# Kernel tuning notes

Hardware: AMD Instinct MI355X
Metric: run time of the kernel (lower is better)

Reference implementation:

```python
import jax, jax.numpy as jnp
import numpy as np

B, N, N_HEAD, HDIM = 16, 512, 8, 64


def setup_inputs() -> dict:
    key = jax.random.key(0)
    kq, kk, kv, kg = jax.random.split(key, 4)
    q = jax.random.normal(kq, (B, N, N_HEAD, HDIM), dtype=jnp.float32)
    k = jax.random.normal(kk, (B, N, N_HEAD, HDIM), dtype=jnp.float32)
    v = jax.random.normal(kv, (B, N, N_HEAD, HDIM), dtype=jnp.float32)
    geo_f = jax.random.normal(kg, (B, N, N), dtype=jnp.float32)
    return {"q": q, "k": k, "v": v, "geo_f": geo_f}


def reference(q, k, v, geo_f):
    # q,k,v: [B,N,H,D]; geo_f: [B,N,N]
    D = q.shape[-1]
    scale = D ** (-0.5)  # total_weight = qk_weight / scale  (i.e. * sqrt(D))
    # pairwise_distance = negative squared Euclidean distance between per-head
    # query/key vectors: -||q_i - k_j||^2 = 2 q.k - ||q||^2 - ||k||^2
    qk = jnp.einsum('bnhd,bmhd->bhnm', q, k)            # [B,H,N,N]
    q2 = jnp.sum(q * q, axis=-1).transpose(0, 2, 1)     # [B,H,N]
    k2 = jnp.sum(k * k, axis=-1).transpose(0, 2, 1)     # [B,H,N]
    dist = 2.0 * qk - q2[..., :, None] - k2[..., None, :]
    total = (dist + geo_f[:, None, :, :]) / scale       # geo bias broadcast over heads
    # global max subtraction in the source is a no-op under softmax; softmax is stable anyway
    w = jax.nn.softmax(total, axis=-1)                  # [B,H,N,N]
    # weighted sum over keys m (dropout p=0.0 -> identity)
    out = jnp.einsum('bmhd,bhnm->bnhd', v, w)           # [B,N,H,D]
    return out
```

## Files before the change

kernel.cpp:

```cpp
#include <hip/hip_runtime.h>
#include <hip/hip_bf16.h>

#define BB 16
#define NN 512
#define NH 8
#define DD 64
#define CK 64
#define NCH 8
#define TL 4
#define MWAVES 8
#define MQBLK 128
#define QBLK 64
#define WAVES 4
#define KBLK 128
#define NCHUNK 4
#define NT 32
#define TPC 8

typedef __attribute__((ext_vector_type(8))) short bf16x8;
typedef __attribute__((ext_vector_type(4))) float f32x4;

__device__ __forceinline__ unsigned short f2bf(float f) {
    unsigned int u = __float_as_uint(f);
    u += 0x7fffu + ((u >> 16) & 1u);
    return (unsigned short)(u >> 16);
}
__device__ __forceinline__ float bf2f(unsigned short h) {
    return __uint_as_float(((unsigned int)h) << 16);
}
__device__ __forceinline__ unsigned int cvtpk(float a, float b) {
    unsigned int r;
    asm("v_cvt_pk_bf16_f32 %0, %1, %2" : "=v"(r) : "v"(a), "v"(b));
    return r;
}
__device__ __forceinline__ void gload16(const void* gsrc, void* lds) {
    __builtin_amdgcn_global_load_lds(
        (const __attribute__((address_space(1))) unsigned int*)gsrc,
        (__attribute__((address_space(3))) unsigned int*)lds, 16, 0, 0);
}

__global__ __launch_bounds__(256) void geo_prep(
    const float* __restrict__ K, const float* __restrict__ V,
    unsigned short* __restrict__ KhiG, unsigned short* __restrict__ KloG,
    unsigned short* __restrict__ VtG, float* __restrict__ k2G)
{
    const int c2 = blockIdx.x;
    const int h  = blockIdx.y;
    const int b  = blockIdx.z;
    const int bh = b*NH + h;
    const int tid = threadIdx.x;
    const int lane16 = tid & 15;
    const int grp    = tid >> 4;

    __shared__ unsigned short Vl[DD*66];

    const size_t kbase = (size_t)bh*(NN*DD) + (size_t)c2*(CK*DD);
    #pragma unroll
    for (int kk = 0; kk < 4; ++kk) {
        const int kl = kk*16 + grp;
        const float* krow = K + ((size_t)(((b*NN + c2*CK + kl)*NH) + h))*DD + lane16*4;
        const float* vrow = V + ((size_t)(((b*NN + c2*CK + kl)*NH) + h))*DD + lane16*4;
        float4 kf = *(const float4*)krow;
        float4 vf = *(const float4*)vrow;
        float fb[4] = {kf.x, kf.y, kf.z, kf.w};
        float vb[4] = {vf.x, vf.y, vf.z, vf.w};
        unsigned short hu[4], lu[4];
        float k2s = 0.f;
        #pragma unroll
        for (int e = 0; e < 4; ++e) {
            float f = fb[e];
            k2s += f*f;
            hu[e] = f2bf(f);
            lu[e] = f2bf(f - bf2f(hu[e]));
            Vl[(lane16*4 + e)*66 + kl] = f2bf(vb[e]);
        }
        k2s += __shfl_xor(k2s, 1);
        k2s += __shfl_xor(k2s, 2);
        k2s += __shfl_xor(k2s, 4);
        k2s += __shfl_xor(k2s, 8);
        if (lane16 == 0) k2G[bh*NN + c2*CK + kl] = -8.f * k2s;
        const int pos = (kl*DD + lane16*4) ^ ((kl & 7) << 3);
        *(uint2*)&KhiG[kbase + pos] = make_uint2((unsigned)hu[0] | ((unsigned)hu[1] << 16),
                                                 (unsigned)hu[2] | ((unsigned)hu[3] << 16));
        *(uint2*)&KloG[kbase + pos] = make_uint2((unsigned)lu[0] | ((unsigned)lu[1] << 16),
                                                 (unsigned)lu[2] | ((unsigned)lu[3] << 16));
    }
    __syncthreads();
    const size_t vbase = ((size_t)bh*NCH + c2)*(DD*CK);
    #pragma unroll
    for (int i = 0; i < 4; ++i) {
        const int gi = tid + 256*i;
        const int d   = gi >> 4;
        const int kl4 = (gi & 15) * 4;
        unsigned short e0 = Vl[d*66 + kl4+0];
        unsigned short e1 = Vl[d*66 + kl4+1];
        unsigned short e2 = Vl[d*66 + kl4+2];
        unsigned short e3 = Vl[d*66 + kl4+3];
        const int pos = (d*CK + kl4) ^ ((d & 7) << 3);
        *(uint2*)&VtG[vbase + pos] = make_uint2((unsigned)e0 | ((unsigned)e1 << 16),
                                                (unsigned)e2 | ((unsigned)e3 << 16));
    }
}

__global__ __launch_bounds__(512, 4) void geo_attn_main(
    const float* __restrict__ Q, const float* __restrict__ GEO,
    const unsigned short* __restrict__ KhiG, const unsigned short* __restrict__ KloG,
    const unsigned short* __restrict__ VtG, const float* __restrict__ k2G,
    float* __restrict__ OUT)
{
    const int bid  = blockIdx.x;
    const int tile = (bid & 7) * 64 + (bid >> 3);
    const int qt = tile & 3;
    const int h  = (tile >> 2) & 7;
    const int b  = tile >> 5;
    const int bh = b*NH + h;
    const int tid = threadIdx.x;
    const int w    = tid >> 6;
    const int lane = tid & 63;
    const int g = lane >> 4;
    const int c = lane & 15;

    __shared__ unsigned short Khi[2][CK*DD];
    __shared__ unsigned short Klo[2][CK*DD];
    __shared__ unsigned short vT [2][CK*DD];
    __shared__ unsigned short Pld[MWAVES*16*CK];
    __shared__ float k2n[NN];

    if (tid < NN) k2n[tid] = k2G[(size_t)bh*NN + tid];

    const int qb = qt*MQBLK + w*16;

    bf16x8 qhi[2], qlo[2];
    {
        const float* qrow = Q + ((size_t)((b*NN + qb + c)*NH + h))*DD;
        #pragma unroll
        for (int dc = 0; dc < 2; ++dc) {
            float buf[8];
            *(float4*)&buf[0] = *(const float4*)(qrow + dc*32 + g*8);
            *(float4*)&buf[4] = *(const float4*)(qrow + dc*32 + g*8 + 4);
            #pragma unroll
            for (int i = 0; i < 8; ++i) {
                float f = buf[i];
                unsigned short hu = f2bf(f);
                qhi[dc][i] = (short)hu;
                qlo[dc][i] = (short)f2bf(f - bf2f(hu));
            }
        }
    }

    f32x4 oacc[4];
    #pragma unroll
    for (int cb = 0; cb < 4; ++cb) { oacc[cb][0]=0.f; oacc[cb][1]=0.f; oacc[cb][2]=0.f; oacc[cb][3]=0.f; }
    float m_run = -3e38f;
    float l_run = 0.f;

    const char* gKhiB = (const char*)KhiG + (size_t)bh*(NN*DD*2);
    const char* gKloB = (const char*)KloG + (size_t)bh*(NN*DD*2);
    const char* gVtB  = (const char*)VtG  + (size_t)bh*(NN*DD*2);
    const float* geoR = GEO + (size_t)b*NN*NN + (size_t)(qb + c)*NN;

    auto stage = [&](int buf, int ch2) {
        const int off = w*1024 + (lane<<4);
        gload16(gKhiB + ch2*(CK*DD*2) + off, (char*)&Khi[buf][0] + w*1024);
        gload16(gKloB + ch2*(CK*DD*2) + off, (char*)&Klo[buf][0] + w*1024);
        gload16(gVtB  + ch2*(CK*DD*2) + off, (char*)&vT [buf][0] + w*1024);
    };

    stage(0, 0);
    __syncthreads();

    for (int ch = 0; ch < NCH; ++ch) {
        const int cur = ch & 1;

        float4 gq[TL];
        #pragma unroll
        for (int tl = 0; tl < TL; ++tl)
            gq[tl] = *(const float4*)(geoR + ch*CK + tl*16 + 4*g);

        if (ch + 1 < NCH) stage(cur ^ 1, ch + 1);

        float4 kn[TL];
        #pragma unroll
        for (int tl = 0; tl < TL; ++tl)
            kn[tl] = *(const float4*)&k2n[ch*CK + tl*16 + 4*g];

        f32x4 sacc[TL];
        #pragma unroll
        for (int tl = 0; tl < TL; ++tl) { sacc[tl][0]=0.f; sacc[tl][1]=0.f; sacc[tl][2]=0.f; sacc[tl][3]=0.f; }
        __builtin_amdgcn_s_setprio(1);
        #pragma unroll
        for (int tl = 0; tl < TL; ++tl) {
            const int key = tl*16 + c;
            #pragma unroll
            for (int dc = 0; dc < 2; ++dc) {
                const int idx = (key*DD + dc*32 + g*8) ^ ((key & 7) << 3);
                bf16x8 kh = *(const bf16x8*)&Khi[cur][idx];
                bf16x8 kl = *(const bf16x8*)&Klo[cur][idx];
                sacc[tl] = __builtin_amdgcn_mfma_f32_16x16x32_bf16(kh, qhi[dc], sacc[tl], 0,0,0);
                sacc[tl] = __builtin_amdgcn_mfma_f32_16x16x32_bf16(kh, qlo[dc], sacc[tl], 0,0,0);
                sacc[tl] = __builtin_amdgcn_mfma_f32_16x16x32_bf16(kl, qhi[dc], sacc[tl], 0,0,0);
            }
        }
        __builtin_amdgcn_s_setprio(0);

        float p[16];
        float cmax = -3e38f;
        #pragma unroll
        for (int tl = 0; tl < TL; ++tl) {
            const float ge[4] = {gq[tl].x, gq[tl].y, gq[tl].z, gq[tl].w};
            const float ke[4] = {kn[tl].x, kn[tl].y, kn[tl].z, kn[tl].w};
            #pragma unroll
            for (int r = 0; r < 4; ++r) {
                float s = fmaf(16.f, sacc[tl][r], fmaf(8.f, ge[r], ke[r]));
                p[tl*4+r] = s;
                cmax = fmaxf(cmax, s);
            }
        }
        cmax = fmaxf(cmax, __shfl_xor(cmax, 16));
        cmax = fmaxf(cmax, __shfl_xor(cmax, 32));
        const float mnew = fmaxf(m_run, cmax);
        const float fac = __expf(m_run - mnew);
        m_run = mnew;
        float cs = 0.f;
        #pragma unroll
        for (int i = 0; i < 16; ++i) { p[i] = __expf(p[i] - mnew); cs += p[i]; }
        cs += __shfl_xor(cs, 16);
        cs += __shfl_xor(cs, 32);
        l_run = fmaf(l_run, fac, cs);

        #pragma unroll
        for (int tl = 0; tl < TL; ++tl) {
            unsigned int u0 = cvtpk(p[tl*4+0], p[tl*4+1]);
            unsigned int u1 = cvtpk(p[tl*4+2], p[tl*4+3]);
            const int idx = (((w*16 + c)*CK) + tl*16 + 4*g) ^ ((c & 7) << 3);
            *(uint2*)&Pld[idx] = make_uint2(u0, u1);
        }

        #pragma unroll
        for (int cb = 0; cb < 4; ++cb) {
            oacc[cb][0] *= fac; oacc[cb][1] *= fac; oacc[cb][2] *= fac; oacc[cb][3] *= fac;
        }
        __builtin_amdgcn_s_setprio(1);
        #pragma unroll
        for (int kc = 0; kc < 2; ++kc) {
            bf16x8 pf = *(const bf16x8*)&Pld[(((w*16 + c)*CK) + kc*32 + g*8) ^ ((c & 7) << 3)];
            #pragma unroll
            for (int cb = 0; cb < 4; ++cb) {
                const int d = cb*16 + c;
                bf16x8 vfr = *(const bf16x8*)&vT[cur][(d*CK + kc*32 + g*8) ^ ((d & 7) << 3)];
                oacc[cb] = __builtin_amdgcn_mfma_f32_16x16x32_bf16(vfr, pf, oacc[cb], 0,0,0);
            }
        }
        __builtin_amdgcn_s_setprio(0);
        __syncthreads();
    }

    const float inv = 1.f / l_run;
    float* orow = OUT + ((size_t)((b*NN + qb + c)*NH + h))*DD + 4*g;
    #pragma unroll
    for (int cb = 0; cb < 4; ++cb) {
        float4 ov;
        ov.x = oacc[cb][0] * inv;
        ov.y = oacc[cb][1] * inv;
        ov.z = oacc[cb][2] * inv;
        ov.w = oacc[cb][3] * inv;
        *(float4*)(orow + cb*16) = ov;
    }
}

__global__ __launch_bounds__(256, 2) void geo_attn_fallback(
    const float* __restrict__ Q, const float* __restrict__ K,
    const float* __restrict__ V, const float* __restrict__ GEO,
    float* __restrict__ OUT)
{
    const int qt  = blockIdx.x;
    const int h   = blockIdx.y;
    const int b   = blockIdx.z;
    const int tid = threadIdx.x;
    const int w    = tid >> 6;
    const int lane = tid & 63;
    const int g = lane >> 4;
    const int c = lane & 15;

    __shared__ unsigned short smemA[16384];
    __shared__ float k2p[2][NN];
    __shared__ float rowinvF[WAVES][16];

    unsigned short* KhiF = smemA;
    unsigned short* KloF = smemA + KBLK*DD;
    unsigned short* vTF  = smemA;
    unsigned short* PldF = smemA + DD*KBLK + w*16*KBLK;

    const int qb = qt*QBLK + w*16;

    bf16x8 qhi[2], qlo[2];
    float q2v = 0.f;
    {
        const float* qrow = Q + ((size_t)((b*NN + qb + c)*NH + h))*DD;
        #pragma unroll
        for (int dc = 0; dc < 2; ++dc) {
            float buf[8];
            *(float4*)&buf[0] = *(const float4*)(qrow + dc*32 + g*8);
            *(float4*)&buf[4] = *(const float4*)(qrow + dc*32 + g*8 + 4);
            #pragma unroll
            for (int i = 0; i < 8; ++i) {
                float f = buf[i];
                q2v += f*f;
                unsigned short hu = f2bf(f);
                qhi[dc][i] = (short)hu;
                qlo[dc][i] = (short)f2bf(f - bf2f(hu));
            }
        }
    }
    q2v += __shfl_xor(q2v, 16);
    q2v += __shfl_xor(q2v, 32);

    f32x4 zero4; zero4[0]=0.f; zero4[1]=0.f; zero4[2]=0.f; zero4[3]=0.f;
    f32x4 acc[NT];
    #pragma unroll
    for (int t = 0; t < NT; ++t) acc[t] = zero4;

    #pragma unroll
    for (int c2 = 0; c2 < NCHUNK; ++c2) {
        __syncthreads();
        {
            const int keyl = tid & (KBLK-1);
            const int half = tid >> 7;
            const int d0 = half*32;
            const float* krow = K + ((size_t)((b*NN + c2*KBLK + keyl)*NH + h))*DD + d0;
            float k2sv = 0.f;
            #pragma unroll
            for (int jj = 0; jj < 8; ++jj) {
                float4 f4 = *(const float4*)(krow + jj*4);
                float fb[4] = {f4.x, f4.y, f4.z, f4.w};
                unsigned short hu[4], lu[4];
                #pragma unroll
                for (int e = 0; e < 4; ++e) {
                    float f = fb[e];
                    k2sv += f*f;
                    hu[e] = f2bf(f);
                    lu[e] = f2bf(f - bf2f(hu[e]));
                }
                int idx = (keyl*DD + d0 + jj*4) ^ ((keyl & 7) << 3);
                *(uint2*)&KhiF[idx] = make_uint2((unsigned)hu[0] | ((unsigned)hu[1] << 16),
                                                 (unsigned)hu[2] | ((unsigned)hu[3] << 16));
                *(uint2*)&KloF[idx] = make_uint2((unsigned)lu[0] | ((unsigned)lu[1] << 16),
                                                 (unsigned)lu[2] | ((unsigned)lu[3] << 16));
            }
            k2p[half][c2*KBLK + keyl] = k2sv;
        }
        __syncthreads();
        #pragma unroll
        for (int tl = 0; tl < TPC; ++tl) {
            const int key = tl*16 + c;
            #pragma unroll
            for (int dc = 0; dc < 2; ++dc) {
                int idx = (key*DD + dc*32 + g*8) ^ ((key & 7) << 3);
                bf16x8 kh = *(const bf16x8*)&KhiF[idx];
                bf16x8 kl = *(const bf16x8*)&KloF[idx];
                acc[c2*TPC+tl] = __builtin_amdgcn_mfma_f32_16x16x32_bf16(qhi[dc], kh, acc[c2*TPC+tl], 0,0,0);
                acc[c2*TPC+tl] = __builtin_amdgcn_mfma_f32_16x16x32_bf16(qlo[dc], kh, acc[c2*TPC+tl], 0,0,0);
                acc[c2*TPC+tl] = __builtin_amdgcn_mfma_f32_16x16x32_bf16(qhi[dc], kl, acc[c2*TPC+tl], 0,0,0);
            }
        }
    }

    float nq2[4];
    #pragma unroll
    for (int r = 0; r < 4; ++r) nq2[r] = -8.f * __shfl(q2v, g*4 + r);

    const float* geoB = GEO + (size_t)b*NN*NN + (size_t)(qb + 4*g)*NN;

    float mx[4] = {-3e38f, -3e38f, -3e38f, -3e38f};
    #pragma unroll
    for (int t = 0; t < NT; ++t) {
        float kk8 = -8.f * (k2p[0][t*16 + c] + k2p[1][t*16 + c]);
        #pragma unroll
        for (int r = 0; r < 4; ++r) {
            float gv = geoB[(size_t)r*NN + t*16 + c];
            float s = fmaf(16.f, acc[t][r], fmaf(8.f, gv, nq2[r] + kk8));
            acc[t][r] = s;
            mx[r] = fmaxf(mx[r], s);
        }
    }
    #pragma unroll
    for (int r = 0; r < 4; ++r) {
        float mv = mx[r];
        mv = fmaxf(mv, __shfl_xor(mv, 1));
        mv = fmaxf(mv, __shfl_xor(mv, 2));
        mv = fmaxf(mv, __shfl_xor(mv, 4));
        mv = fmaxf(mv, __shfl_xor(mv, 8));
        mx[r] = mv;
    }
    float sm[4] = {0.f, 0.f, 0.f, 0.f};
    #pragma unroll
    for (int t = 0; t < NT; ++t) {
        #pragma unroll
        for (int r = 0; r < 4; ++r) {
            float p = __expf(acc[t][r] - mx[r]);
            acc[t][r] = p;
            sm[r] += p;
        }
    }
    #pragma unroll
    for (int r = 0; r < 4; ++r) {
        float sv = sm[r];
        sv += __shfl_xor(sv, 1);
        sv += __shfl_xor(sv, 2);
        sv += __shfl_xor(sv, 4);
        sv += __shfl_xor(sv, 8);
        sm[r] = sv;
    }
    if (c == 0) {
        #pragma unroll
        for (int r = 0; r < 4; ++r) rowinvF[w][4*g + r] = 1.f / sm[r];
    }

    f32x4 oacc[4];
    #pragma unroll
    for (int cb = 0; cb < 4; ++cb) oacc[cb] = zero4;

    #pragma unroll
    for (int c2 = 0; c2 < NCHUNK; ++c2) {
        __syncthreads();
        {
            const int keyl = tid & (KBLK-1);
            const int half = tid >> 7;
            const int d0 = half*32;
            const float* vrow = V + ((size_t)((b*NN + c2*KBLK + keyl)*NH + h))*DD + d0;
            #pragma unroll
            for (int jj = 0; jj < 8; ++jj) {
                float4 f4 = *(const float4*)(vrow + jj*4);
                float fb[4] = {f4.x, f4.y, f4.z, f4.w};
                #pragma unroll
                for (int e = 0; e < 4; ++e) {
                    int d = d0 + jj*4 + e;
                    vTF[(d*KBLK + keyl) ^ ((d & 7) << 3)] = f2bf(fb[e]);
                }
            }
        }
        #pragma unroll
        for (int tl = 0; tl < TPC; ++tl) {
            #pragma unroll
            for (int r = 0; r < 4; ++r) {
                int qloc = 4*g + r;
                PldF[(qloc*KBLK + tl*16 + c) ^ ((qloc & 7) << 3)] = f2bf(acc[c2*TPC+tl][r]);
            }
        }
        __syncthreads();
        #pragma unroll
        for (int kc = 0; kc < 4; ++kc) {
            int kb2 = kc*32 + g*8;
            bf16x8 pf = *(const bf16x8*)&PldF[(c*KBLK + kb2) ^ ((c & 7) << 3)];
            #pragma unroll
            for (int cb = 0; cb < 4; ++cb) {
                int d = cb*16 + c;
                bf16x8 vf = *(const bf16x8*)&vTF[(d*KBLK + kb2) ^ ((d & 7) << 3)];
                oacc[cb] = __builtin_amdgcn_mfma_f32_16x16x32_bf16(vf, pf, oacc[cb], 0,0,0);
            }
        }
    }

    const float inv = rowinvF[w][c];
    float* orow = OUT + ((size_t)((b*NN + qb + c)*NH + h))*DD + 4*g;
    #pragma unroll
    for (int cb = 0; cb < 4; ++cb) {
        float4 ov;
        ov.x = oacc[cb][0] * inv;
        ov.y = oacc[cb][1] * inv;
        ov.z = oacc[cb][2] * inv;
        ov.w = oacc[cb][3] * inv;
        *(float4*)(orow + cb*16) = ov;
    }
}

extern "C" void kernel_launch(void* const* d_in, const int* in_sizes, int n_in,
                              void* d_out, int out_size, void* d_ws, size_t ws_size,
                              hipStream_t stream) {
    const float* q   = (const float*)d_in[0];
    const float* k   = (const float*)d_in[1];
    const float* v   = (const float*)d_in[2];
    const float* geo = (const float*)d_in[3];
    float* out = (float*)d_out;

    const size_t IMG = (size_t)BB*NH*NN*DD*2;
    const size_t need = 3*IMG + (size_t)BB*NH*NN*4;

    if (ws_size >= need) {
        unsigned short* KhiG = (unsigned short*)d_ws;
        unsigned short* KloG = (unsigned short*)((char*)d_ws + IMG);
        unsigned short* VtG  = (unsigned short*)((char*)d_ws + 2*IMG);
        float*          k2G  = (float*)((char*)d_ws + 3*IMG);
        dim3 pgrid(NCH, NH, BB);
        geo_prep<<<pgrid, 256, 0, stream>>>(k, v, KhiG, KloG, VtG, k2G);
        geo_attn_main<<<dim3(512), 512, 0, stream>>>(q, geo, KhiG, KloG, VtG, k2G, out);
    } else {
        dim3 grid(NN/QBLK, NH, BB);
        geo_attn_fallback<<<grid, 256, 0, stream>>>(q, k, v, geo, out);
    }
}
```

Before: 132.8 us.

## Keep softmax probabilities in registers via permuted K layout, use exp2

Reorders keys in the preprocessed K layout so the MFMA score output lanes line up with the B-operand layout of the PV MFMA. The probabilities can then be packed straight into bf16x8 registers, removing the shared-memory P round trip. Scales are folded so exp2 replaces exp, and the max and sum reductions become trees. The main loop is unrolled by two with geo loads prefetched one chunk ahead. The layout change ties the preprocessing and attention kernels together, so any mismatch in the permutation would give wrong results.

```diff
diff --git a/kernel.cpp b/kernel.cpp
--- a/kernel.cpp
+++ b/kernel.cpp
@@ -17,6 +17,10 @@
 #define NT 32
 #define TPC 8
 
+#define LOG2E  1.4426950408889634f
+#define C_QK   23.083120654223414f
+#define C_GEO  11.541560327111707f
+
 typedef __attribute__((ext_vector_type(8))) short bf16x8;
 typedef __attribute__((ext_vector_type(4))) float f32x4;
 
@@ -78,8 +82,9 @@
         k2s += __shfl_xor(k2s, 2);
         k2s += __shfl_xor(k2s, 4);
         k2s += __shfl_xor(k2s, 8);
-        if (lane16 == 0) k2G[bh*NN + c2*CK + kl] = -8.f * k2s;
-        const int pos = (kl*DD + lane16*4) ^ ((kl & 7) << 3);
+        if (lane16 == 0) k2G[bh*NN + c2*CK + kl] = -C_GEO * k2s;
+        const int j = 16*(((kl & 7) >> 2) + 2*(kl >> 5)) + 4*((kl >> 3) & 3) + (kl & 3);
+        const int pos = (j*DD + lane16*4) ^ ((j & 7) << 3);
         *(uint2*)&KhiG[kbase + pos] = make_uint2((unsigned)hu[0] | ((unsigned)hu[1] << 16),
                                                  (unsigned)hu[2] | ((unsigned)hu[3] << 16));
         *(uint2*)&KloG[kbase + pos] = make_uint2((unsigned)lu[0] | ((unsigned)lu[1] << 16),
@@ -123,10 +128,9 @@
     __shared__ unsigned short Khi[2][CK*DD];
     __shared__ unsigned short Klo[2][CK*DD];
     __shared__ unsigned short vT [2][CK*DD];
-    __shared__ unsigned short Pld[MWAVES*16*CK];
     __shared__ float k2n[NN];
 
-    if (tid < NN) k2n[tid] = k2G[(size_t)bh*NN + tid];
+    k2n[tid] = k2G[(size_t)bh*NN + tid];
 
     const int qb = qt*MQBLK + w*16;
 
@@ -165,24 +169,17 @@
         gload16(gKloB + ch2*(CK*DD*2) + off, (char*)&Klo[buf][0] + w*1024);
         gload16(gVtB  + ch2*(CK*DD*2) + off, (char*)&vT [buf][0] + w*1024);
     };
-
-    stage(0, 0);
-    __syncthreads();
-
-    for (int ch = 0; ch < NCH; ++ch) {
-        const int cur = ch & 1;
-
-        float4 gq[TL];
+    auto loadgeo = [&](float4 (&dst)[TL], int ch) {
         #pragma unroll
         for (int tl = 0; tl < TL; ++tl)
-            gq[tl] = *(const float4*)(geoR + ch*CK + tl*16 + 4*g);
-
-        if (ch + 1 < NCH) stage(cur ^ 1, ch + 1);
-
+            dst[tl] = *(const float4*)(geoR + ch*CK + 32*(tl>>1) + 8*g + 4*(tl&1));
+    };
+
+    auto compute = [&](int ch, int cur, float4 (&gq)[TL]) {
         float4 kn[TL];
         #pragma unroll
         for (int tl = 0; tl < TL; ++tl)
-            kn[tl] = *(const float4*)&k2n[ch*CK + tl*16 + 4*g];
+            kn[tl] = *(const float4*)&k2n[ch*CK + 32*(tl>>1) + 8*g + 4*(tl&1)];
 
         f32x4 sacc[TL];
         #pragma unroll
@@ -190,10 +187,9 @@
         __builtin_amdgcn_s_setprio(1);
         #pragma unroll
         for (int tl = 0; tl < TL; ++tl) {
-            const int key = tl*16 + c;
             #pragma unroll
             for (int dc = 0; dc < 2; ++dc) {
-                const int idx = (key*DD + dc*32 + g*8) ^ ((key & 7) << 3);
+                const int idx = ((tl*16 + c)*DD + dc*32 + g*8) ^ ((c & 7) << 3);
                 bf16x8 kh = *(const bf16x8*)&Khi[cur][idx];
                 bf16x8 kl = *(const bf16x8*)&Klo[cur][idx];
                 sacc[tl] = __builtin_amdgcn_mfma_f32_16x16x32_bf16(kh, qhi[dc], sacc[tl], 0,0,0);
@@ -204,37 +200,43 @@
         __builtin_amdgcn_s_setprio(0);
 
         float p[16];
-        float cmax = -3e38f;
         #pragma unroll
         for (int tl = 0; tl < TL; ++tl) {
             const float ge[4] = {gq[tl].x, gq[tl].y, gq[tl].z, gq[tl].w};
             const float ke[4] = {kn[tl].x, kn[tl].y, kn[tl].z, kn[tl].w};
             #pragma unroll
-            for (int r = 0; r < 4; ++r) {
-                float s = fmaf(16.f, sacc[tl][r], fmaf(8.f, ge[r], ke[r]));
-                p[tl*4+r] = s;
-                cmax = fmaxf(cmax, s);
-            }
-        }
+            for (int r = 0; r < 4; ++r)
+                p[tl*4+r] = fmaf(C_QK, sacc[tl][r], fmaf(C_GEO, ge[r], ke[r]));
+        }
+        float mx[8];
+        #pragma unroll
+        for (int i = 0; i < 8; ++i) mx[i] = fmaxf(p[i], p[i+8]);
+        #pragma unroll
+        for (int i = 0; i < 4; ++i) mx[i] = fmaxf(mx[i], mx[i+4]);
+        mx[0] = fmaxf(mx[0], mx[2]); mx[1] = fmaxf(mx[1], mx[3]);
+        float cmax = fmaxf(mx[0], mx[1]);
         cmax = fmaxf(cmax, __shfl_xor(cmax, 16));
         cmax = fmaxf(cmax, __shfl_xor(cmax, 32));
         const float mnew = fmaxf(m_run, cmax);
-        const float fac = __expf(m_run - mnew);
+        const float fac = exp2f(m_run - mnew);
         m_run = mnew;
-        float cs = 0.f;
-        #pragma unroll
-        for (int i = 0; i < 16; ++i) { p[i] = __expf(p[i] - mnew); cs += p[i]; }
+        #pragma unroll
+        for (int i = 0; i < 16; ++i) p[i] = exp2f(p[i] - mnew);
+        float sx[8];
+        #pragma unroll
+        for (int i = 0; i < 8; ++i) sx[i] = p[i] + p[i+8];
+        #pragma unroll
+        for (int i = 0; i < 4; ++i) sx[i] = sx[i] + sx[i+4];
+        float cs = (sx[0] + sx[2]) + (sx[1] + sx[3]);
         cs += __shfl_xor(cs, 16);
         cs += __shfl_xor(cs, 32);
         l_run = fmaf(l_run, fac, cs);
 
-        #pragma unroll
-        for (int tl = 0; tl < TL; ++tl) {
-            unsigned int u0 = cvtpk(p[tl*4+0], p[tl*4+1]);
-            unsigned int u1 = cvtpk(p[tl*4+2], p[tl*4+3]);
-            const int idx = (((w*16 + c)*CK) + tl*16 + 4*g) ^ ((c & 7) << 3);
-            *(uint2*)&Pld[idx] = make_uint2(u0, u1);
-        }
+        union { unsigned int u[4]; bf16x8 v; } pf0, pf1;
+        pf0.u[0] = cvtpk(p[0], p[1]);  pf0.u[1] = cvtpk(p[2],  p[3]);
+        pf0.u[2] = cvtpk(p[4], p[5]);  pf0.u[3] = cvtpk(p[6],  p[7]);
+        pf1.u[0] = cvtpk(p[8], p[9]);  pf1.u[1] = cvtpk(p[10], p[11]);
+        pf1.u[2] = cvtpk(p[12],p[13]); pf1.u[3] = cvtpk(p[14], p[15]);
 
         #pragma unroll
         for (int cb = 0; cb < 4; ++cb) {
@@ -243,7 +245,7 @@
         __builtin_amdgcn_s_setprio(1);
         #pragma unroll
         for (int kc = 0; kc < 2; ++kc) {
-            bf16x8 pf = *(const bf16x8*)&Pld[(((w*16 + c)*CK) + kc*32 + g*8) ^ ((c & 7) << 3)];
+            bf16x8 pf = kc ? pf1.v : pf0.v;
             #pragma unroll
             for (int cb = 0; cb < 4; ++cb) {
                 const int d = cb*16 + c;
@@ -252,6 +254,24 @@
             }
         }
         __builtin_amdgcn_s_setprio(0);
+    };
+
+    float4 gqA[TL], gqB[TL];
+    stage(0, 0);
+    loadgeo(gqA, 0);
+    __syncthreads();
+
+    for (int cc = 0; cc < 4; ++cc) {
+        const int ch0 = cc*2;
+        stage(1, ch0 + 1);
+        loadgeo(gqB, ch0 + 1);
+        compute(ch0, 0, gqA);
+        __syncthreads();
+        if (cc < 3) {
+            stage(0, ch0 + 2);
+            loadgeo(gqA, ch0 + 2);
+        }
+        compute(ch0 + 1, 1, gqB);
         __syncthreads();
     }
 
```

Result: slower. 169.3 us (+27.5%).

## Permute K rows so P stays in registers, use exp2 and prefetch geo

Applied to the files above, without the earlier changes.

The prep kernel now writes K rows in a permuted order. Each lane's score accumulators then line up directly with the B-operand layout of the PV MFMA, so the P tile goes straight from registers into bf16 fragments and the LDS round-trip through Pld is gone. Softmax constants are folded into log2 scale so the exponential can use the raw v_exp_f32 instruction. Row sums are kept per lane and reduced once at the end instead of on every chunk. The chunk loop is manually unrolled with geo loads for the next chunk issued ahead of compute, which raises register pressure.

```diff
diff --git a/kernel.cpp b/kernel.cpp
--- a/kernel.cpp
+++ b/kernel.cpp
@@ -17,6 +17,9 @@
 #define NT 32
 #define TPC 8
 
+#define C_QK   23.083120654223414f
+#define C_GEO  11.541560327111707f
+
 typedef __attribute__((ext_vector_type(8))) short bf16x8;
 typedef __attribute__((ext_vector_type(4))) float f32x4;
 
@@ -31,6 +34,11 @@
 __device__ __forceinline__ unsigned int cvtpk(float a, float b) {
     unsigned int r;
     asm("v_cvt_pk_bf16_f32 %0, %1, %2" : "=v"(r) : "v"(a), "v"(b));
+    return r;
+}
+__device__ __forceinline__ float exp2fast(float x) {
+    float r;
+    asm("v_exp_f32 %0, %1" : "=v"(r) : "v"(x));
     return r;
 }
 __device__ __forceinline__ void gload16(const void* gsrc, void* lds) {
@@ -78,8 +86,9 @@
         k2s += __shfl_xor(k2s, 2);
         k2s += __shfl_xor(k2s, 4);
         k2s += __shfl_xor(k2s, 8);
-        if (lane16 == 0) k2G[bh*NN + c2*CK + kl] = -8.f * k2s;
-        const int pos = (kl*DD + lane16*4) ^ ((kl & 7) << 3);
+        if (lane16 == 0) k2G[bh*NN + c2*CK + kl] = -C_GEO * k2s;
+        const int j = 16*(((kl & 7) >> 2) + 2*(kl >> 5)) + 4*((kl >> 3) & 3) + (kl & 3);
+        const int pos = (j*DD + lane16*4) ^ ((j & 7) << 3);
         *(uint2*)&KhiG[kbase + pos] = make_uint2((unsigned)hu[0] | ((unsigned)hu[1] << 16),
                                                  (unsigned)hu[2] | ((unsigned)hu[3] << 16));
         *(uint2*)&KloG[kbase + pos] = make_uint2((unsigned)lu[0] | ((unsigned)lu[1] << 16),
@@ -123,10 +132,9 @@
     __shared__ unsigned short Khi[2][CK*DD];
     __shared__ unsigned short Klo[2][CK*DD];
     __shared__ unsigned short vT [2][CK*DD];
-    __shared__ unsigned short Pld[MWAVES*16*CK];
     __shared__ float k2n[NN];
 
-    if (tid < NN) k2n[tid] = k2G[(size_t)bh*NN + tid];
+    k2n[tid] = k2G[(size_t)bh*NN + tid];
 
     const int qb = qt*MQBLK + w*16;
 
@@ -158,103 +166,128 @@
     const char* gKloB = (const char*)KloG + (size_t)bh*(NN*DD*2);
     const char* gVtB  = (const char*)VtG  + (size_t)bh*(NN*DD*2);
     const float* geoR = GEO + (size_t)b*NN*NN + (size_t)(qb + c)*NN;
-
-    auto stage = [&](int buf, int ch2) {
-        const int off = w*1024 + (lane<<4);
-        gload16(gKhiB + ch2*(CK*DD*2) + off, (char*)&Khi[buf][0] + w*1024);
-        gload16(gKloB + ch2*(CK*DD*2) + off, (char*)&Klo[buf][0] + w*1024);
-        gload16(gVtB  + ch2*(CK*DD*2) + off, (char*)&vT [buf][0] + w*1024);
-    };
-
-    stage(0, 0);
+    const int stoff = w*1024 + (lane<<4);
+
+#define STAGE(BUF, CH2) {                                                        \
+    const size_t srcoff = (size_t)(CH2)*(CK*DD*2) + stoff;                       \
+    gload16(gKhiB + srcoff, (char*)&Khi[BUF][0] + w*1024);                       \
+    gload16(gKloB + srcoff, (char*)&Klo[BUF][0] + w*1024);                       \
+    gload16(gVtB  + srcoff, (char*)&vT [BUF][0] + w*1024);                       \
+}
+#define LOAD_GEO(CH, D0, D1, D2, D3) {                                           \
+    const float* gb_ = geoR + (CH)*CK + 8*g;                                     \
+    D0 = *(const float4*)(gb_);                                                  \
+    D1 = *(const float4*)(gb_ + 4);                                              \
+    D2 = *(const float4*)(gb_ + 32);                                             \
+    D3 = *(const float4*)(gb_ + 36);                                             \
+}
+#define COMPUTE(CH, CUR, G0, G1, G2, G3) {                                       \
+    f32x4 sacc[TL];                                                              \
+    _Pragma("unroll")                                                            \
+    for (int tl = 0; tl < TL; ++tl) { sacc[tl][0]=0.f; sacc[tl][1]=0.f; sacc[tl][2]=0.f; sacc[tl][3]=0.f; } \
+    __builtin_amdgcn_s_setprio(1);                                               \
+    _Pragma("unroll")                                                            \
+    for (int tl = 0; tl < TL; ++tl) {                                            \
+        _Pragma("unroll")                                                        \
+        for (int dc = 0; dc < 2; ++dc) {                                         \
+            const int idx = ((tl*16 + c)*DD + dc*32 + g*8) ^ ((c & 7) << 3);     \
+            bf16x8 kh = *(const bf16x8*)&Khi[CUR][idx];                          \
+            bf16x8 kl = *(const bf16x8*)&Klo[CUR][idx];                          \
+            sacc[tl] = __builtin_amdgcn_mfma_f32_16x16x32_bf16(kh, qhi[dc], sacc[tl], 0,0,0); \
+            sacc[tl] = __builtin_amdgcn_mfma_f32_16x16x32_bf16(kh, qlo[dc], sacc[tl], 0,0,0); \
+            sacc[tl] = __builtin_amdgcn_mfma_f32_16x16x32_bf16(kl, qhi[dc], sacc[tl], 0,0,0); \
+        }                                                                        \
+    }                                                                            \
+    __builtin_amdgcn_s_setprio(0);                                               \
+    const float4 kn0 = *(const float4*)&k2n[(CH)*CK + 8*g];                      \
+    const float4 kn1 = *(const float4*)&k2n[(CH)*CK + 8*g + 4];                  \
+    const float4 kn2 = *(const float4*)&k2n[(CH)*CK + 8*g + 32];                 \
+    const float4 kn3 = *(const float4*)&k2n[(CH)*CK + 8*g + 36];                 \
+    float p[16];                                                                 \
+    p[0]  = fmaf(C_QK, sacc[0][0], fmaf(C_GEO, G0.x, kn0.x));                    \
+    p[1]  = fmaf(C_QK, sacc[0][1], fmaf(C_GEO, G0.y, kn0.y));                    \
+    p[2]  = fmaf(C_QK, sacc[0][2], fmaf(C_GEO, G0.z, kn0.z));                    \
+    p[3]  = fmaf(C_QK, sacc[0][3], fmaf(C_GEO, G0.w, kn0.w));                    \
+    p[4]  = fmaf(C_QK, sacc[1][0], fmaf(C_GEO, G1.x, kn1.x));                    \
+    p[5]  = fmaf(C_QK, sacc[1][1], fmaf(C_GEO, G1.y, kn1.y));                    \
+    p[6]  = fmaf(C_QK, sacc[1][2], fmaf(C_GEO, G1.z, kn1.z));                    \
+    p[7]  = fmaf(C_QK, sacc[1][3], fmaf(C_GEO, G1.w, kn1.w));                    \
+    p[8]  = fmaf(C_QK, sacc[2][0], fmaf(C_GEO, G2.x, kn2.x));                    \
+    p[9]  = fmaf(C_QK, sacc[2][1], fmaf(C_GEO, G2.y, kn2.y));                    \
+    p[10] = fmaf(C_QK, sacc[2][2], fmaf(C_GEO, G2.z, kn2.z));                    \
+    p[11] = fmaf(C_QK, sacc[2][3], fmaf(C_GEO, G2.w, kn2.w));                    \
+    p[12] = fmaf(C_QK, sacc[3][0], fmaf(C_GEO, G3.x, kn3.x));                    \
+    p[13] = fmaf(C_QK, sacc[3][1], fmaf(C_GEO, G3.y, kn3.y));                    \
+    p[14] = fmaf(C_QK, sacc[3][2], fmaf(C_GEO, G3.z, kn3.z));                    \
+    p[15] = fmaf(C_QK, sacc[3][3], fmaf(C_GEO, G3.w, kn3.w));                    \
+    float mx[8];                                                                 \
+    _Pragma("unroll")                                                            \
+    for (int i = 0; i < 8; ++i) mx[i] = fmaxf(p[i], p[i+8]);                     \
+    _Pragma("unroll")                                                            \
+    for (int i = 0; i < 4; ++i) mx[i] = fmaxf(mx[i], mx[i+4]);                   \
+    mx[0] = fmaxf(mx[0], mx[2]); mx[1] = fmaxf(mx[1], mx[3]);                    \
+    float cmax = fmaxf(mx[0], mx[1]);                                            \
+    cmax = fmaxf(cmax, __shfl_xor(cmax, 16));                                    \
+    cmax = fmaxf(cmax, __shfl_xor(cmax, 32));                                    \
+    const float mnew = fmaxf(m_run, cmax);                                       \
+    const float fac = exp2fast(m_run - mnew);                                    \
+    m_run = mnew;                                                                \
+    _Pragma("unroll")                                                            \
+    for (int i = 0; i < 16; ++i) p[i] = exp2fast(p[i] - mnew);                   \
+    float sx[8];                                                                 \
+    _Pragma("unroll")                                                            \
+    for (int i = 0; i < 8; ++i) sx[i] = p[i] + p[i+8];                           \
+    _Pragma("unroll")                                                            \
+    for (int i = 0; i < 4; ++i) sx[i] = sx[i] + sx[i+4];                         \
+    const float cs = (sx[0] + sx[2]) + (sx[1] + sx[3]);                          \
+    l_run = fmaf(l_run, fac, cs);       \
+    union { unsigned int u[4]; bf16x8 v; } pf0, pf1;                             \
+    pf0.u[0] = cvtpk(p[0], p[1]);  pf0.u[1] = cvtpk(p[2],  p[3]);                \
+    pf0.u[2] = cvtpk(p[4], p[5]);  pf0.u[3] = cvtpk(p[6],  p[7]);                \
+    pf1.u[0] = cvtpk(p[8], p[9]);  pf1.u[1] = cvtpk(p[10], p[11]);               \
+    pf1.u[2] = cvtpk(p[12],p[13]); pf1.u[3] = cvtpk(p[14], p[15]);               \
+    _Pragma("unroll")                                                            \
+    for (int cb = 0; cb < 4; ++cb) {                                             \
+        oacc[cb][0] *= fac; oacc[cb][1] *= fac; oacc[cb][2] *= fac; oacc[cb][3] *= fac; \
+    }                                                                            \
+    __builtin_amdgcn_s_setprio(1);                                               \
+    _Pragma("unroll")                                                            \
+    for (int kc = 0; kc < 2; ++kc) {                                             \
+        bf16x8 pf = kc ? pf1.v : pf0.v;                                          \
+        _Pragma("unroll")                                                        \
+        for (int cb = 0; cb < 4; ++cb) {                                         \
+            const int d = cb*16 + c;                                             \
+            bf16x8 vfr = *(const bf16x8*)&vT[CUR][(d*CK + kc*32 + g*8) ^ ((d & 7) << 3)]; \
+            oacc[cb] = __builtin_amdgcn_mfma_f32_16x16x32_bf16(vfr, pf, oacc[cb], 0,0,0); \
+        }                                                                        \
+    }                                                                            \
+    __builtin_amdgcn_s_setprio(0);                                               \
+}
+
+    float4 gA0, gA1, gA2, gA3;
+    float4 gB0, gB1, gB2, gB3;
+
+    STAGE(0, 0);
+    LOAD_GEO(0, gA0, gA1, gA2, gA3);
     __syncthreads();
 
-    for (int ch = 0; ch < NCH; ++ch) {
-        const int cur = ch & 1;
-
-        float4 gq[TL];
-        #pragma unroll
-        for (int tl = 0; tl < TL; ++tl)
-            gq[tl] = *(const float4*)(geoR + ch*CK + tl*16 + 4*g);
-
-        if (ch + 1 < NCH) stage(cur ^ 1, ch + 1);
-
-        float4 kn[TL];
-        #pragma unroll
-        for (int tl = 0; tl < TL; ++tl)
-            kn[tl] = *(const float4*)&k2n[ch*CK + tl*16 + 4*g];
-
-        f32x4 sacc[TL];
-        #pragma unroll
-        for (int tl = 0; tl < TL; ++tl) { sacc[tl][0]=0.f; sacc[tl][1]=0.f; sacc[tl][2]=0.f; sacc[tl][3]=0.f; }
-        __builtin_amdgcn_s_setprio(1);
-        #pragma unroll
-        for (int tl = 0; tl < TL; ++tl) {
-            const int key = tl*16 + c;
-            #pragma unroll
-            for (int dc = 0; dc < 2; ++dc) {
-                const int idx = (key*DD + dc*32 + g*8) ^ ((key & 7) << 3);
-                bf16x8 kh = *(const bf16x8*)&Khi[cur][idx];
-                bf16x8 kl = *(const bf16x8*)&Klo[cur][idx];
-                sacc[tl] = __builtin_amdgcn_mfma_f32_16x16x32_bf16(kh, qhi[dc], sacc[tl], 0,0,0);
-                sacc[tl] = __builtin_amdgcn_mfma_f32_16x16x32_bf16(kh, qlo[dc], sacc[tl], 0,0,0);
-                sacc[tl] = __builtin_amdgcn_mfma_f32_16x16x32_bf16(kl, qhi[dc], sacc[tl], 0,0,0);
-            }
-        }
-        __builtin_amdgcn_s_setprio(0);
-
-        float p[16];
-        float cmax = -3e38f;
-        #pragma unroll
-        for (int tl = 0; tl < TL; ++tl) {
-            const float ge[4] = {gq[tl].x, gq[tl].y, gq[tl].z, gq[tl].w};
-            const float ke[4] = {kn[tl].x, kn[tl].y, kn[tl].z, kn[tl].w};
-            #pragma unroll
-            for (int r = 0; r < 4; ++r) {
-                float s = fmaf(16.f, sacc[tl][r], fmaf(8.f, ge[r], ke[r]));
-                p[tl*4+r] = s;
-                cmax = fmaxf(cmax, s);
-            }
-        }
-        cmax = fmaxf(cmax, __shfl_xor(cmax, 16));
-        cmax = fmaxf(cmax, __shfl_xor(cmax, 32));
-        const float mnew = fmaxf(m_run, cmax);
-        const float fac = __expf(m_run - mnew);
-        m_run = mnew;
-        float cs = 0.f;
-        #pragma unroll
-        for (int i = 0; i < 16; ++i) { p[i] = __expf(p[i] - mnew); cs += p[i]; }
-        cs += __shfl_xor(cs, 16);
-        cs += __shfl_xor(cs, 32);
-        l_run = fmaf(l_run, fac, cs);
-
-        #pragma unroll
-        for (int tl = 0; tl < TL; ++tl) {
-            unsigned int u0 = cvtpk(p[tl*4+0], p[tl*4+1]);
-            unsigned int u1 = cvtpk(p[tl*4+2], p[tl*4+3]);
-            const int idx = (((w*16 + c)*CK) + tl*16 + 4*g) ^ ((c & 7) << 3);
-            *(uint2*)&Pld[idx] = make_uint2(u0, u1);
-        }
-
-        #pragma unroll
-        for (int cb = 0; cb < 4; ++cb) {
-            oacc[cb][0] *= fac; oacc[cb][1] *= fac; oacc[cb][2] *= fac; oacc[cb][3] *= fac;
-        }
-        __builtin_amdgcn_s_setprio(1);
-        #pragma unroll
-        for (int kc = 0; kc < 2; ++kc) {
-            bf16x8 pf = *(const bf16x8*)&Pld[(((w*16 + c)*CK) + kc*32 + g*8) ^ ((c & 7) << 3)];
-            #pragma unroll
-            for (int cb = 0; cb < 4; ++cb) {
-                const int d = cb*16 + c;
-                bf16x8 vfr = *(const bf16x8*)&vT[cur][(d*CK + kc*32 + g*8) ^ ((d & 7) << 3)];
-                oacc[cb] = __builtin_amdgcn_mfma_f32_16x16x32_bf16(vfr, pf, oacc[cb], 0,0,0);
-            }
-        }
-        __builtin_amdgcn_s_setprio(0);
+    #pragma unroll
+    for (int cc = 0; cc < 4; ++cc) {
+        const int ch0 = cc*2;
+        STAGE(1, ch0 + 1);
+        LOAD_GEO(ch0 + 1, gB0, gB1, gB2, gB3);
+        COMPUTE(ch0, 0, gA0, gA1, gA2, gA3);
         __syncthreads();
-    }
-
+        if (cc < 3) {
+            STAGE(0, ch0 + 2);
+            LOAD_GEO(ch0 + 2, gA0, gA1, gA2, gA3);
+        }
+        COMPUTE(ch0 + 1, 1, gB0, gB1, gB2, gB3);
+        __syncthreads();
+    }
+
+    l_run += __shfl_xor(l_run, 16);
+    l_run += __shfl_xor(l_run, 32);
     const float inv = 1.f / l_run;
     float* orow = OUT + ((size_t)((b*NN + qb + c)*NH + h))*DD + 4*g;
     #pragma unroll
@@ -266,6 +299,9 @@
         ov.w = oacc[cb][3] * inv;
         *(float4*)(orow + cb*16) = ov;
     }
+#undef STAGE
+#undef LOAD_GEO
+#undef COMPUTE
 }
 
 __global__ __launch_bounds__(256, 2) void geo_attn_fallback(
```

Measured after the change: 173.2 us. +30.4%, slower.
